# Optimization experiments

Measured on AMD Instinct MI355X. Metric: run time of the kernel, lower is better.

## Reference

```python
import jax, jax.numpy as jnp
from jax import lax
import numpy as np

VOCAB, E, H, T = 8000, 300, 75, 6  # H = hidden_dim//2 per direction
B, S = 256, 512
START, STOP = 4, 5
NEG = -10000.0


def setup_inputs() -> dict:
    key = jax.random.key(0)
    ks = jax.random.split(key, 16)
    sc = 0.1  # keep activations in sane range
    trans = jax.random.normal(ks[14], (T, T), jnp.float32)
    trans = trans.at[START, :].set(NEG).at[:, STOP].set(NEG)
    return {
        "sentence": jax.random.randint(ks[0], (B, S), 0, VOCAB),
        "tags": jax.random.randint(ks[1], (B, S), 0, 4),  # only B/I/E/S gold tags
        "embedding": jax.random.normal(ks[2], (VOCAB, E), jnp.float32),
        "w_ih_f": sc * jax.random.normal(ks[3], (4 * H, E), jnp.float32),
        "w_hh_f": sc * jax.random.normal(ks[4], (4 * H, H), jnp.float32),
        "b_ih_f": sc * jax.random.normal(ks[5], (4 * H,), jnp.float32),
        "b_hh_f": sc * jax.random.normal(ks[6], (4 * H,), jnp.float32),
        "w_ih_b": sc * jax.random.normal(ks[7], (4 * H, E), jnp.float32),
        "w_hh_b": sc * jax.random.normal(ks[8], (4 * H, H), jnp.float32),
        "b_ih_b": sc * jax.random.normal(ks[9], (4 * H,), jnp.float32),
        "b_hh_b": sc * jax.random.normal(ks[10], (4 * H,), jnp.float32),
        "h0": jax.random.normal(ks[11], (2, B, H), jnp.float32),
        "c0": jax.random.normal(ks[12], (2, B, H), jnp.float32),
        "w_out": sc * jax.random.normal(ks[13], (T, 2 * H), jnp.float32),
        "b_out": sc * jax.random.normal(ks[15], (T,), jnp.float32),
        "transitions": trans,
    }


def _lstm_dir(xg, w_hh, h0, c0, reverse):
    # xg: [S, B, 4H] precomputed input gates; PyTorch gate order i, f, g, o
    def step(carry, g):
        h, c = carry
        gates = g + h @ w_hh.T
        i, f, gg, o = jnp.split(gates, 4, axis=-1)
        c = jax.nn.sigmoid(f) * c + jax.nn.sigmoid(i) * jnp.tanh(gg)
        h = jax.nn.sigmoid(o) * jnp.tanh(c)
        return (h, c), h

    _, hs = lax.scan(step, (h0, c0), xg, reverse=reverse)
    return hs  # [S, B, H]


def reference(sentence, tags, embedding, w_ih_f, w_hh_f, b_ih_f, b_hh_f,
              w_ih_b, w_hh_b, b_ih_b, b_hh_b, h0, c0, w_out, b_out, transitions):
    # --- BiLSTM features ---
    embeds = embedding[sentence].transpose(1, 0, 2)  # [S, B, E]
    xg_f = embeds @ w_ih_f.T + (b_ih_f + b_hh_f)
    xg_b = embeds @ w_ih_b.T + (b_ih_b + b_hh_b)
    hf = _lstm_dir(xg_f, w_hh_f, h0[0], c0[0], reverse=False)
    hb = _lstm_dir(xg_b, w_hh_b, h0[1], c0[1], reverse=True)
    lstm_out = jnp.concatenate([hf, hb], axis=-1)  # [S, B, 2H]
    feats = lstm_out @ w_out.T + b_out  # [S, B, T]

    # --- CRF forward algorithm (log partition) ---
    alpha0 = jnp.full((feats.shape[1], T), NEG, feats.dtype).at[:, START].set(0.0)

    def crf_step(alpha, feat):
        # alpha_new[b, j] = logsumexp_i(alpha[b, i] + trans[j, i] + feat[b, j])
        alpha = jax.nn.logsumexp(
            alpha[:, None, :] + transitions[None, :, :] + feat[:, :, None], axis=2)
        return alpha, None

    alpha, _ = lax.scan(crf_step, alpha0, feats)
    forward_score = jax.nn.logsumexp(alpha + transitions[STOP][None, :], axis=1)  # [B]

    # --- gold path score ---
    tags_ext = jnp.concatenate(
        [jnp.full((tags.shape[0], 1), START, tags.dtype), tags], axis=1)  # [B, S+1]
    trans_sc = transitions[tags_ext[:, 1:], tags_ext[:, :-1]].sum(axis=1)  # [B]
    feats_bt = feats.transpose(1, 0, 2)  # [B, S, T]
    emit_sc = jnp.take_along_axis(feats_bt, tags[:, :, None], axis=2)[..., 0].sum(axis=1)
    gold_score = trans_sc + emit_sc + transitions[STOP, tags[:, -1]]

    return forward_score - gold_score  # [B] per-sentence CRF NLL
```

## Files before the change

kernel.cpp:

```cpp
#include <hip/hip_runtime.h>
#include <stdint.h>

#define VOCABN 8000
#define EE     300
#define HH     75
#define G4     300
#define TT     6
#define BB     256
#define SS     512
#define STARTT 4
#define STOPT  5
#define NEGV   (-10000.0f)
#define NCH    16
#define CHL    32

typedef __fp16 fp16x2 __attribute__((ext_vector_type(2)));
typedef __fp16 f16x8 __attribute__((ext_vector_type(8)));
typedef float f32x4 __attribute__((ext_vector_type(4)));
typedef unsigned int u32;

__device__ __forceinline__ float sigf(float x){
  return __builtin_amdgcn_rcpf(1.0f + __expf(-x));
}
__device__ __forceinline__ float tanhf_(float x){
  return __builtin_fmaf(__builtin_amdgcn_rcpf(1.0f + __expf(-2.0f * x)), 2.0f, -1.0f);
}
__device__ __forceinline__ float pk2(float a, float b){
  fp16x2 r = __builtin_amdgcn_cvt_pkrtz(a, b);
  return __builtin_bit_cast(float, r);
}
__device__ __forceinline__ float dot2pk(float a, float b, float c){
  asm("v_dot2_f32_f16 %0, %1, %2, %0" : "+v"(c) : "v"(a), "v"(b));
  return c;
}
__device__ __forceinline__ void sync_lds(){
  __builtin_amdgcn_sched_barrier(0);
  asm volatile("s_waitcnt lgkmcnt(0)" ::: "memory");
  __builtin_amdgcn_s_barrier();
  __builtin_amdgcn_sched_barrier(0);
}

__global__ __launch_bounds__(256) void k_gemm(
    const float* __restrict__ emb, const float* __restrict__ w_ih_f,
    const float* __restrict__ w_ih_b,
    const float* __restrict__ b_ih_f, const float* __restrict__ b_hh_f,
    const float* __restrict__ b_ih_b, const float* __restrict__ b_hh_b,
    float* __restrict__ vxg){
  __shared__ alignas(16) __fp16 bfrag[19 * 64 * 8];
  __shared__ float bias_sh[304];
  const int bx = blockIdx.x;
  const int dir = bx / 125;
  const int vblk = bx % 125;
  const int v0 = vblk * 64;
  const int tid = threadIdx.x;
  const int w = tid >> 6, lane = tid & 63;
  const int bb = lane & 15, q = lane >> 4;
  const float* wdir = dir ? w_ih_b : w_ih_f;

  for (int g = tid; g < 304; g += 256){
    float bi = 0.f;
    if (g < G4){
      int gs = (g & 3) * 75 + (g >> 2);
      bi = dir ? (b_ih_b[gs] + b_hh_b[gs]) : (b_ih_f[gs] + b_hh_f[gs]);
    }
    bias_sh[g] = bi;
  }
  if (tid < 16){
    int col = 12 + (tid & 3), qq = tid >> 2;
    *(u32*)&bfrag[(18 * 64 + qq * 16 + col) * 8]     = 0;
    *(u32*)&bfrag[(18 * 64 + qq * 16 + col) * 8 + 2] = 0;
    *(u32*)&bfrag[(18 * 64 + qq * 16 + col) * 8 + 4] = 0;
    *(u32*)&bfrag[(18 * 64 + qq * 16 + col) * 8 + 6] = 0;
  }

  f32x4 acc[19];
  #pragma unroll
  for (int t = 0; t < 19; ++t) acc[t] = (f32x4){0.f, 0.f, 0.f, 0.f};

  const float* arow = emb + (size_t)(v0 + 16 * w + bb) * EE;
  const int rstage = tid >> 3;
  const int sub = tid & 7;

  for (int c = 0; c < 10; ++c){
    f16x8 afrag;
    const int kb = 32 * c + 8 * q;
    if (c < 9){
      float4 x0 = *(const float4*)(arow + kb);
      float4 x1 = *(const float4*)(arow + kb + 4);
      afrag[0] = (__fp16)x0.x; afrag[1] = (__fp16)x0.y;
      afrag[2] = (__fp16)x0.z; afrag[3] = (__fp16)x0.w;
      afrag[4] = (__fp16)x1.x; afrag[5] = (__fp16)x1.y;
      afrag[6] = (__fp16)x1.z; afrag[7] = (__fp16)x1.w;
    } else {
      #pragma unroll
      for (int j = 0; j < 8; ++j)
        afrag[j] = (kb + j < EE) ? (__fp16)arow[kb + j] : (__fp16)0.f;
    }

    __syncthreads();
    for (int r0 = 0; r0 < 300; r0 += 32){
      int r = r0 + rstage;
      if (r < 300){
        int gsrc2 = (r & 3) * 75 + (r >> 2);
        const float* wr = wdir + (size_t)gsrc2 * EE;
        int e0 = 32 * c + 4 * sub;
        float4 xv;
        if (e0 + 3 < EE) xv = *(const float4*)(wr + e0);
        else {
          xv.x = (e0     < EE) ? wr[e0]     : 0.f;
          xv.y = (e0 + 1 < EE) ? wr[e0 + 1] : 0.f;
          xv.z = (e0 + 2 < EE) ? wr[e0 + 2] : 0.f;
          xv.w = (e0 + 3 < EE) ? wr[e0 + 3] : 0.f;
        }
        fp16x2 lo = __builtin_amdgcn_cvt_pkrtz(xv.x, xv.y);
        fp16x2 hi = __builtin_amdgcn_cvt_pkrtz(xv.z, xv.w);
        int t2 = r >> 4, col = r & 15;
        int qq = sub >> 1, j = 4 * (sub & 1);
        u32* dst = (u32*)&bfrag[(t2 * 64 + qq * 16 + col) * 8 + j];
        dst[0] = __builtin_bit_cast(u32, lo);
        dst[1] = __builtin_bit_cast(u32, hi);
      }
    }
    __syncthreads();

    #pragma unroll
    for (int t = 0; t < 19; ++t){
      f16x8 bf = *(const f16x8*)&bfrag[(t * 64 + lane) * 8];
      asm("v_mfma_f32_16x16x32_f16 %0, %1, %2, %0"
          : "+v"(acc[t]) : "v"(afrag), "v"(bf));
    }
  }

  const size_t obase = (size_t)dir * VOCABN * G4;
  #pragma unroll
  for (int t = 0; t < 19; ++t){
    int g = 16 * t + bb;
    if (g < G4){
      float bi = bias_sh[g];
      #pragma unroll
      for (int r = 0; r < 4; ++r){
        int v = v0 + 16 * w + 4 * q + r;
        vxg[obase + (size_t)v * G4 + g] = acc[t][r] + bi;
      }
    }
  }
}

__global__ __launch_bounds__(640) void k_lstm(
    const int* __restrict__ sentence, const float* __restrict__ vxg,
    const float* __restrict__ w_hh_f, const float* __restrict__ w_hh_b,
    const float* __restrict__ h0, const float* __restrict__ c0,
    const float* __restrict__ w_out, const float* __restrict__ b_out,
    float* __restrict__ featsF, float* __restrict__ featsB){
  __shared__ int tok_sh[SS * 16];
  __shared__ alignas(16) __fp16 hfrag[2][12 * 16 * 8];
  const int bx = blockIdx.x;
  const int dir = bx >> 4, group = bx & 15;
  const int t = threadIdx.x;
  const int w = t >> 6, lane = t & 63;
  const int bb = lane & 15, q = lane >> 4;
  const int T0 = 2 * w, T1 = 2 * w + 1;
  const int rbA = 16 * T0 + 4 * q, rbB = 16 * T1 + 4 * q;
  const int hA = rbA >> 2, hB = rbB >> 2;
  const int bglob = group * 16 + bb;
  const int wiA = w * 128 + bb * 8 + q;
  const int wiB = w * 128 + bb * 8 + 4 + q;

  for (int i = t; i < 2 * 12 * 16 * 4; i += 640) ((u32*)hfrag)[i] = 0;
  for (int i = t; i < 16 * SS; i += 640){
    int bq = i >> 9, s = i & 511;
    tok_sh[s * 16 + ((bq + s) & 15)] = sentence[(size_t)(group * 16 + bq) * SS + s];
  }
  __syncthreads();

  const float* whh = dir ? w_hh_b : w_hh_f;
  f16x8 a00, a01, a02, a10, a11, a12;
  #define BUILD_A(dst, T, c) { \
    int m = 16 * (T) + bb; int kb = 32 * (c) + 8 * q; \
    _Pragma("unroll") \
    for (int j = 0; j < 8; ++j){ \
      int kk = kb + j; float wv = 0.f; \
      if (kk < HH){ \
        if (m < 300) wv = whh[((m & 3) * 75 + (m >> 2)) * HH + kk]; \
        else if (m < 306) wv = w_out[(m - 300) * (2 * HH) + dir * HH + kk]; \
      } \
      dst[j] = (__fp16)wv; } }
  BUILD_A(a00, T0, 0) BUILD_A(a01, T0, 1) BUILD_A(a02, T0, 2)
  BUILD_A(a10, T1, 0) BUILD_A(a11, T1, 1) BUILD_A(a12, T1, 2)

  float cA = 0.f, cB = 0.f;
  if (hA < HH){
    cA = c0[((size_t)dir * BB + bglob) * HH + hA];
    hfrag[0][wiA] = (__fp16)h0[((size_t)dir * BB + bglob) * HH + hA];
  }
  if (hB < HH){
    cB = c0[((size_t)dir * BB + bglob) * HH + hB];
    hfrag[0][wiB] = (__fp16)h0[((size_t)dir * BB + bglob) * HH + hB];
  }
  const float bo0 = dir ? 0.f : b_out[0], bo1 = dir ? 0.f : b_out[1];
  const float bo2 = dir ? 0.f : b_out[2], bo3 = dir ? 0.f : b_out[3];
  const float bo4 = dir ? 0.f : b_out[4], bo5 = dir ? 0.f : b_out[5];
  __syncthreads();

  const float* vx = vxg + (size_t)dir * VOCABN * G4;
  float* feats = dir ? featsB : featsF;
  const float4 zf4 = {0.f, 0.f, 0.f, 0.f};

#define LOADXG(d0, d1, kstep) { \
    if ((kstep) < SS){ \
      int sr_ = dir ? (SS - 1 - (kstep)) : (kstep); \
      int tk_ = tok_sh[sr_ * 16 + ((bb + sr_) & 15)]; \
      const float* base_ = vx + (size_t)tk_ * G4; \
      d0 = (hA < HH) ? *(const float4*)(base_ + rbA) : zf4; \
      d1 = (hB < HH) ? *(const float4*)(base_ + rbB) : zf4; \
    } else { d0 = zf4; d1 = zf4; } }

  float4 cur0, cur1, n10, n11, n20, n21, n30, n31, p0, p1;
  LOADXG(cur0, cur1, 0)
  LOADXG(n10, n11, 1)
  LOADXG(n20, n21, 2)
  LOADXG(n30, n31, 3)

  for (int k = 0; k <= SS; ++k){
    const __fp16* hq = hfrag[k & 1];
    f16x8 b0 = *(const f16x8*)&hq[(0 * 64 + lane) * 8];
    f16x8 b1 = *(const f16x8*)&hq[(1 * 64 + lane) * 8];
    f16x8 b2 = *(const f16x8*)&hq[(2 * 64 + lane) * 8];

    LOADXG(p0, p1, k + 4)

    f32x4 acc0 = {cur0.x, cur0.y, cur0.z, cur0.w};
    f32x4 acc1 = {cur1.x, cur1.y, cur1.z, cur1.w};
    asm("v_mfma_f32_16x16x32_f16 %0, %1, %2, %0" : "+v"(acc0) : "a"(a00), "v"(b0));
    asm("v_mfma_f32_16x16x32_f16 %0, %1, %2, %0" : "+v"(acc1) : "a"(a10), "v"(b0));
    asm("v_mfma_f32_16x16x32_f16 %0, %1, %2, %0" : "+v"(acc0) : "a"(a01), "v"(b1));
    asm("v_mfma_f32_16x16x32_f16 %0, %1, %2, %0" : "+v"(acc1) : "a"(a11), "v"(b1));
    asm("v_mfma_f32_16x16x32_f16 %0, %1, %2, %0" : "+v"(acc0) : "a"(a02), "v"(b2));
    asm("v_mfma_f32_16x16x32_f16 %0, %1, %2, %0" : "+v"(acc1) : "a"(a12), "v"(b2));

    __fp16* hw = hfrag[(k & 1) ^ 1];
    if (k < SS){
      if (hA < HH){
        float gi = acc0.x, gf = acc0.y, gg = acc0.z, go = acc0.w;
        cA = sigf(gf) * cA + sigf(gi) * tanhf_(gg);
        hw[wiA] = (__fp16)(sigf(go) * tanhf_(cA));
      }
      if (hB < HH){
        float gi = acc1.x, gf = acc1.y, gg = acc1.z, go = acc1.w;
        cB = sigf(gf) * cB + sigf(gi) * tanhf_(gg);
        hw[wiB] = (__fp16)(sigf(go) * tanhf_(cB));
      }
    }
    if (k >= 1){
      if (rbA == 300){
        int ps = dir ? (SS - k) : (k - 1);
        float* fb = feats + ((size_t)ps * BB + bglob) * TT;
        float2 v01 = {acc0.x + bo0, acc0.y + bo1};
        float2 v23 = {acc0.z + bo2, acc0.w + bo3};
        *(float2*)fb = v01;
        *(float2*)(fb + 2) = v23;
      }
      if (rbB == 304){
        int ps = dir ? (SS - k) : (k - 1);
        float* fb = feats + ((size_t)ps * BB + bglob) * TT;
        float2 v45 = {acc1.x + bo4, acc1.y + bo5};
        *(float2*)(fb + 4) = v45;
      }
    }
    cur0 = n10; cur1 = n11;
    n10 = n20;  n11 = n21;
    n20 = n30;  n21 = n31;
    n30 = p0;   n31 = p1;
    sync_lds();
  }
}

#define LOADSTAGE(X0,X1,X2,Y0,Y1,Y2, srow) do{ \
  int _r = (srow); if (_r >= SS) _r = 0; \
  const float2* _pF = (const float2*)(featsF + ((size_t)_r * BB + b) * TT); \
  const float2* _pB = (const float2*)(featsB + ((size_t)_r * BB + b) * TT); \
  X0 = _pF[0]; X1 = _pF[1]; X2 = _pF[2]; \
  Y0 = _pB[0]; Y1 = _pB[1]; Y2 = _pB[2]; }while(0)

#define ASTEP(X0,X1,X2,Y0,Y1,Y2, srow) do{ \
  float F0 = X0.x + Y0.x, F1 = X0.y + Y0.y, F2 = X1.x + Y1.x; \
  float F3 = X1.y + Y1.y, F4 = X2.x + Y2.x, F5 = X2.y + Y2.y; \
  float M = fmaxf(fmaxf(fmaxf(a0,a1),fmaxf(a2,a3)),fmaxf(a4,a5)); \
  float p01 = pk2(__expf(a0-M), __expf(a1-M)); \
  float p23 = pk2(__expf(a2-M), __expf(a3-M)); \
  float p45 = pk2(__expf(a4-M), __expf(a5-M)); \
  float s0 = dot2pk(p45, Tq2,  dot2pk(p23, Tq1,  dot2pk(p01, Tq0,  0.f))); \
  float s1 = dot2pk(p45, Tq5,  dot2pk(p23, Tq4,  dot2pk(p01, Tq3,  0.f))); \
  float s2 = dot2pk(p45, Tq8,  dot2pk(p23, Tq7,  dot2pk(p01, Tq6,  0.f))); \
  float s3 = dot2pk(p45, Tq11, dot2pk(p23, Tq10, dot2pk(p01, Tq9,  0.f))); \
  float s4 = dot2pk(p45, Tq14, dot2pk(p23, Tq13, dot2pk(p01, Tq12, 0.f))); \
  float s5 = dot2pk(p45, Tq17, dot2pk(p23, Tq16, dot2pk(p01, Tq15, 0.f))); \
  a0 = M + __logf(fmaxf(s0, 1e-37f)) + F0;  a1 = M + __logf(fmaxf(s1, 1e-37f)) + F1; \
  a2 = M + __logf(fmaxf(s2, 1e-37f)) + F2;  a3 = M + __logf(fmaxf(s3, 1e-37f)) + F3; \
  a4 = M + __logf(fmaxf(s4, 1e-37f)) + F4;  a5 = M + __logf(fmaxf(s5, 1e-37f)) + F5; \
  LOADSTAGE(X0,X1,X2,Y0,Y1,Y2, (srow) + 2); }while(0)

__global__ __launch_bounds__(256) void k_crf_scan(
    const float* __restrict__ featsF, const float* __restrict__ featsB,
    const float* __restrict__ trans, const int* __restrict__ tags,
    float* __restrict__ crfM, float* __restrict__ pgold){
  __shared__ float tr_sh[36];
  __shared__ u32 etp_sh[18];
  const int tid = threadIdx.x;
  if (tid < 36) tr_sh[tid] = trans[tid];
  if (tid < 18) etp_sh[tid] = __float_as_uint(
      pk2(__expf(trans[2 * tid]), __expf(trans[2 * tid + 1])));
  __syncthreads();
  const int bx = blockIdx.x;

  if (bx < 96){
    const int g = bx * 256 + tid;
    const int s0i = g % 6;
    const int c = (g / 6) % NCH;
    const int b = g / (6 * NCH);
    const int cbase = c * CHL;

    float Tq0=__int_as_float(etp_sh[0]),  Tq1=__int_as_float(etp_sh[1]),
          Tq2=__int_as_float(etp_sh[2]),  Tq3=__int_as_float(etp_sh[3]),
          Tq4=__int_as_float(etp_sh[4]),  Tq5=__int_as_float(etp_sh[5]),
          Tq6=__int_as_float(etp_sh[6]),  Tq7=__int_as_float(etp_sh[7]),
          Tq8=__int_as_float(etp_sh[8]),  Tq9=__int_as_float(etp_sh[9]),
          Tq10=__int_as_float(etp_sh[10]), Tq11=__int_as_float(etp_sh[11]),
          Tq12=__int_as_float(etp_sh[12]), Tq13=__int_as_float(etp_sh[13]),
          Tq14=__int_as_float(etp_sh[14]), Tq15=__int_as_float(etp_sh[15]),
          Tq16=__int_as_float(etp_sh[16]), Tq17=__int_as_float(etp_sh[17]);

    float a0 = (s0i == 0) ? 0.f : NEGV, a1 = (s0i == 1) ? 0.f : NEGV;
    float a2 = (s0i == 2) ? 0.f : NEGV, a3 = (s0i == 3) ? 0.f : NEGV;
    float a4 = (s0i == 4) ? 0.f : NEGV, a5 = (s0i == 5) ? 0.f : NEGV;

    float2 xA0,xA1,xA2,yA0,yA1,yA2, xB0,xB1,xB2,yB0,yB1,yB2;
    LOADSTAGE(xA0,xA1,xA2,yA0,yA1,yA2, cbase + 0);
    LOADSTAGE(xB0,xB1,xB2,yB0,yB1,yB2, cbase + 1);
    for (int s = 0; s < CHL; s += 2){
      ASTEP(xA0,xA1,xA2,yA0,yA1,yA2, cbase + s);
      ASTEP(xB0,xB1,xB2,yB0,yB1,yB2, cbase + s + 1);
    }
    float* mrow = crfM + ((size_t)(b * NCH + c) * 6 + s0i) * 6;
    mrow[0] = a0; mrow[1] = a1; mrow[2] = a2;
    mrow[3] = a3; mrow[4] = a4; mrow[5] = a5;
  } else {
    const int g2 = (bx - 96) * 256 + tid;
    const int b = g2 / NCH;
    const int c = g2 % NCH;
    const int* tg = tags + (size_t)b * SS + c * CHL;
    int prev = (c == 0) ? STARTT : tg[-1];
    float acc = 0.f;
    #pragma unroll 4
    for (int s = 0; s < CHL; ++s){
      int ct = tg[s];
      size_t fo = (size_t)(c * CHL + s) * BB * TT + (size_t)b * TT + ct;
      acc += tr_sh[ct * 6 + prev] + featsF[fo] + featsB[fo];
      prev = ct;
    }
    pgold[b * NCH + c] = acc;
  }
}

__global__ __launch_bounds__(64) void k_crf_comb(
    const float* __restrict__ crfM, const float* __restrict__ pgold,
    const float* __restrict__ trans, const int* __restrict__ tags,
    float* __restrict__ out){
  const int b = blockIdx.x * 64 + threadIdx.x;
  float v0 = NEGV, v1 = NEGV, v2 = NEGV, v3 = NEGV, v4 = 0.f, v5 = NEGV;
  for (int c = 0; c < NCH; ++c){
    const float* mb = crfM + (size_t)(b * NCH + c) * 36;
    float n[6];
    #pragma unroll
    for (int j = 0; j < 6; ++j){
      float t0 = v0 + mb[0 * 6 + j], t1 = v1 + mb[1 * 6 + j];
      float t2 = v2 + mb[2 * 6 + j], t3 = v3 + mb[3 * 6 + j];
      float t4 = v4 + mb[4 * 6 + j], t5 = v5 + mb[5 * 6 + j];
      float m = fmaxf(fmaxf(fmaxf(t0,t1),fmaxf(t2,t3)),fmaxf(t4,t5));
      float s = __expf(t0-m)+__expf(t1-m)+__expf(t2-m)
              + __expf(t3-m)+__expf(t4-m)+__expf(t5-m);
      n[j] = m + __logf(s);
    }
    v0 = n[0]; v1 = n[1]; v2 = n[2]; v3 = n[3]; v4 = n[4]; v5 = n[5];
  }
  float z0 = v0 + trans[30], z1 = v1 + trans[31], z2 = v2 + trans[32];
  float z3 = v3 + trans[33], z4 = v4 + trans[34], z5 = v5 + trans[35];
  float M2 = fmaxf(fmaxf(fmaxf(z0,z1),fmaxf(z2,z3)),fmaxf(z4,z5));
  float ss = __expf(z0-M2)+__expf(z1-M2)+__expf(z2-M2)
           + __expf(z3-M2)+__expf(z4-M2)+__expf(z5-M2);
  float fwd = M2 + __logf(ss);

  float gold = trans[STOPT * 6 + tags[(size_t)b * SS + SS - 1]];
  #pragma unroll
  for (int c = 0; c < NCH; ++c) gold += pgold[b * NCH + c];
  out[b] = fwd - gold;
}

extern "C" void kernel_launch(void* const* d_in, const int* in_sizes, int n_in,
                              void* d_out, int out_size, void* d_ws, size_t ws_size,
                              hipStream_t stream){
  const int*   sentence = (const int*)  d_in[0];
  const int*   tags     = (const int*)  d_in[1];
  const float* emb      = (const float*)d_in[2];
  const float* w_ih_f   = (const float*)d_in[3];
  const float* w_hh_f   = (const float*)d_in[4];
  const float* b_ih_f   = (const float*)d_in[5];
  const float* b_hh_f   = (const float*)d_in[6];
  const float* w_ih_b   = (const float*)d_in[7];
  const float* w_hh_b   = (const float*)d_in[8];
  const float* b_ih_b   = (const float*)d_in[9];
  const float* b_hh_b   = (const float*)d_in[10];
  const float* h0       = (const float*)d_in[11];
  const float* c0       = (const float*)d_in[12];
  const float* w_out    = (const float*)d_in[13];
  const float* b_out    = (const float*)d_in[14];
  const float* trans    = (const float*)d_in[15];
  float* out = (float*)d_out;

  float* ws = (float*)d_ws;
  float* vxg    = ws;
  float* featsF = vxg + (size_t)2 * VOCABN * G4;
  float* featsB = featsF + (size_t)SS * BB * TT;
  float* crfM   = featsB + (size_t)SS * BB * TT;
  float* pgold  = crfM + (size_t)BB * NCH * 36;

  k_gemm<<<2 * 125, 256, 0, stream>>>(emb, w_ih_f, w_ih_b,
                                      b_ih_f, b_hh_f, b_ih_b, b_hh_b, vxg);
  k_lstm<<<32, 640, 0, stream>>>(sentence, vxg, w_hh_f, w_hh_b, h0, c0, w_out, b_out,
                                 featsF, featsB);
  k_crf_scan<<<96 + 16, 256, 0, stream>>>(featsF, featsB, trans, tags, crfM, pgold);
  k_crf_comb<<<BB / 64, 64, 0, stream>>>(crfM, pgold, trans, tags, out);
}
```

Measured before the change: 467.6 us.

## Process two 16-sequence batch slices per LSTM block to interleave recurrences

Each LSTM block now handles 32 batch rows as two independent 16-row slices, so the grid drops from 32 to 16 blocks. The two recurrences interleave their MFMAs and gate math, which can hide MFMA and transcendental latency on the serial step chain. Token indices are stored as u16 to fit twice as many in LDS, and the xg prefetch depth falls from 4 steps to 2 to save registers. The risk is a longer per-step critical path (twice the MFMAs and activations per wave), fewer CUs in use, and more exposed global-load latency from the shallower prefetch.

Result: slower. 815.2 us (+74.3%).

```diff
diff --git a/kernel.cpp b/kernel.cpp
--- a/kernel.cpp
+++ b/kernel.cpp
@@ -18,6 +18,7 @@
 typedef __fp16 f16x8 __attribute__((ext_vector_type(8)));
 typedef float f32x4 __attribute__((ext_vector_type(4)));
 typedef unsigned int u32;
+typedef unsigned short u16;
 
 __device__ __forceinline__ float sigf(float x){
   return __builtin_amdgcn_rcpf(1.0f + __expf(-x));
@@ -152,24 +153,26 @@
     const float* __restrict__ h0, const float* __restrict__ c0,
     const float* __restrict__ w_out, const float* __restrict__ b_out,
     float* __restrict__ featsF, float* __restrict__ featsB){
-  __shared__ int tok_sh[SS * 16];
-  __shared__ alignas(16) __fp16 hfrag[2][12 * 16 * 8];
+  __shared__ u16 tok_sh[SS * 32];
+  __shared__ alignas(16) __fp16 hfrag[2][2][12 * 16 * 8];
   const int bx = blockIdx.x;
-  const int dir = bx >> 4, group = bx & 15;
+  const int dir = bx >> 3, group = bx & 7;
   const int t = threadIdx.x;
   const int w = t >> 6, lane = t & 63;
   const int bb = lane & 15, q = lane >> 4;
   const int T0 = 2 * w, T1 = 2 * w + 1;
   const int rbA = 16 * T0 + 4 * q, rbB = 16 * T1 + 4 * q;
   const int hA = rbA >> 2, hB = rbB >> 2;
-  const int bglob = group * 16 + bb;
+  const int bg0 = group * 32 + bb;
+  const int bg1 = group * 32 + 16 + bb;
   const int wiA = w * 128 + bb * 8 + q;
   const int wiB = w * 128 + bb * 8 + 4 + q;
 
-  for (int i = t; i < 2 * 12 * 16 * 4; i += 640) ((u32*)hfrag)[i] = 0;
-  for (int i = t; i < 16 * SS; i += 640){
+  for (int i = t; i < 2 * 2 * 12 * 16 * 4; i += 640) ((u32*)hfrag)[i] = 0;
+  for (int i = t; i < 32 * SS; i += 640){
     int bq = i >> 9, s = i & 511;
-    tok_sh[s * 16 + ((bq + s) & 15)] = sentence[(size_t)(group * 16 + bq) * SS + s];
+    tok_sh[s * 32 + ((bq + s) & 31)] =
+        (u16)sentence[(size_t)(group * 32 + bq) * SS + s];
   }
   __syncthreads();
 
@@ -188,14 +191,18 @@
   BUILD_A(a00, T0, 0) BUILD_A(a01, T0, 1) BUILD_A(a02, T0, 2)
   BUILD_A(a10, T1, 0) BUILD_A(a11, T1, 1) BUILD_A(a12, T1, 2)
 
-  float cA = 0.f, cB = 0.f;
+  float cA0 = 0.f, cB0 = 0.f, cA1 = 0.f, cB1 = 0.f;
   if (hA < HH){
-    cA = c0[((size_t)dir * BB + bglob) * HH + hA];
-    hfrag[0][wiA] = (__fp16)h0[((size_t)dir * BB + bglob) * HH + hA];
+    cA0 = c0[((size_t)dir * BB + bg0) * HH + hA];
+    cA1 = c0[((size_t)dir * BB + bg1) * HH + hA];
+    hfrag[0][0][wiA] = (__fp16)h0[((size_t)dir * BB + bg0) * HH + hA];
+    hfrag[0][1][wiA] = (__fp16)h0[((size_t)dir * BB + bg1) * HH + hA];
   }
   if (hB < HH){
-    cB = c0[((size_t)dir * BB + bglob) * HH + hB];
-    hfrag[0][wiB] = (__fp16)h0[((size_t)dir * BB + bglob) * HH + hB];
+    cB0 = c0[((size_t)dir * BB + bg0) * HH + hB];
+    cB1 = c0[((size_t)dir * BB + bg1) * HH + hB];
+    hfrag[0][0][wiB] = (__fp16)h0[((size_t)dir * BB + bg0) * HH + hB];
+    hfrag[0][1][wiB] = (__fp16)h0[((size_t)dir * BB + bg1) * HH + hB];
   }
   const float bo0 = dir ? 0.f : b_out[0], bo1 = dir ? 0.f : b_out[1];
   const float bo2 = dir ? 0.f : b_out[2], bo3 = dir ? 0.f : b_out[3];
@@ -206,71 +213,96 @@
   float* feats = dir ? featsB : featsF;
   const float4 zf4 = {0.f, 0.f, 0.f, 0.f};
 
-#define LOADXG(d0, d1, kstep) { \
+#define LOADXG2(dA0, dB0, dA1, dB1, kstep) { \
     if ((kstep) < SS){ \
       int sr_ = dir ? (SS - 1 - (kstep)) : (kstep); \
-      int tk_ = tok_sh[sr_ * 16 + ((bb + sr_) & 15)]; \
-      const float* base_ = vx + (size_t)tk_ * G4; \
-      d0 = (hA < HH) ? *(const float4*)(base_ + rbA) : zf4; \
-      d1 = (hB < HH) ? *(const float4*)(base_ + rbB) : zf4; \
-    } else { d0 = zf4; d1 = zf4; } }
-
-  float4 cur0, cur1, n10, n11, n20, n21, n30, n31, p0, p1;
-  LOADXG(cur0, cur1, 0)
-  LOADXG(n10, n11, 1)
-  LOADXG(n20, n21, 2)
-  LOADXG(n30, n31, 3)
+      int tk0_ = tok_sh[sr_ * 32 + ((bb + sr_) & 31)]; \
+      int tk1_ = tok_sh[sr_ * 32 + ((bb + 16 + sr_) & 31)]; \
+      const float* bs0_ = vx + (size_t)tk0_ * G4; \
+      const float* bs1_ = vx + (size_t)tk1_ * G4; \
+      dA0 = (hA < HH) ? *(const float4*)(bs0_ + rbA) : zf4; \
+      dB0 = (hB < HH) ? *(const float4*)(bs0_ + rbB) : zf4; \
+      dA1 = (hA < HH) ? *(const float4*)(bs1_ + rbA) : zf4; \
+      dB1 = (hB < HH) ? *(const float4*)(bs1_ + rbB) : zf4; \
+    } else { dA0 = zf4; dB0 = zf4; dA1 = zf4; dB1 = zf4; } }
+
+  float4 curA0, curB0, curA1, curB1, nxA0, nxB0, nxA1, nxB1;
+  float4 pA0, pB0, pA1, pB1;
+  LOADXG2(curA0, curB0, curA1, curB1, 0)
+  LOADXG2(nxA0, nxB0, nxA1, nxB1, 1)
 
   for (int k = 0; k <= SS; ++k){
-    const __fp16* hq = hfrag[k & 1];
-    f16x8 b0 = *(const f16x8*)&hq[(0 * 64 + lane) * 8];
-    f16x8 b1 = *(const f16x8*)&hq[(1 * 64 + lane) * 8];
-    f16x8 b2 = *(const f16x8*)&hq[(2 * 64 + lane) * 8];
-
-    LOADXG(p0, p1, k + 4)
-
-    f32x4 acc0 = {cur0.x, cur0.y, cur0.z, cur0.w};
-    f32x4 acc1 = {cur1.x, cur1.y, cur1.z, cur1.w};
-    asm("v_mfma_f32_16x16x32_f16 %0, %1, %2, %0" : "+v"(acc0) : "a"(a00), "v"(b0));
-    asm("v_mfma_f32_16x16x32_f16 %0, %1, %2, %0" : "+v"(acc1) : "a"(a10), "v"(b0));
-    asm("v_mfma_f32_16x16x32_f16 %0, %1, %2, %0" : "+v"(acc0) : "a"(a01), "v"(b1));
-    asm("v_mfma_f32_16x16x32_f16 %0, %1, %2, %0" : "+v"(acc1) : "a"(a11), "v"(b1));
-    asm("v_mfma_f32_16x16x32_f16 %0, %1, %2, %0" : "+v"(acc0) : "a"(a02), "v"(b2));
-    asm("v_mfma_f32_16x16x32_f16 %0, %1, %2, %0" : "+v"(acc1) : "a"(a12), "v"(b2));
-
-    __fp16* hw = hfrag[(k & 1) ^ 1];
+    const __fp16* hq0 = hfrag[k & 1][0];
+    const __fp16* hq1 = hfrag[k & 1][1];
+    f16x8 b0s0 = *(const f16x8*)&hq0[(0 * 64 + lane) * 8];
+    f16x8 b0s1 = *(const f16x8*)&hq1[(0 * 64 + lane) * 8];
+    f16x8 b1s0 = *(const f16x8*)&hq0[(1 * 64 + lane) * 8];
+    f16x8 b1s1 = *(const f16x8*)&hq1[(1 * 64 + lane) * 8];
+    f16x8 b2s0 = *(const f16x8*)&hq0[(2 * 64 + lane) * 8];
+    f16x8 b2s1 = *(const f16x8*)&hq1[(2 * 64 + lane) * 8];
+
+    LOADXG2(pA0, pB0, pA1, pB1, k + 2)
+
+    f32x4 accA0 = {curA0.x, curA0.y, curA0.z, curA0.w};
+    f32x4 accA1 = {curA1.x, curA1.y, curA1.z, curA1.w};
+    f32x4 accB0 = {curB0.x, curB0.y, curB0.z, curB0.w};
+    f32x4 accB1 = {curB1.x, curB1.y, curB1.z, curB1.w};
+    asm("v_mfma_f32_16x16x32_f16 %0, %1, %2, %0" : "+v"(accA0) : "a"(a00), "v"(b0s0));
+    asm("v_mfma_f32_16x16x32_f16 %0, %1, %2, %0" : "+v"(accA1) : "a"(a00), "v"(b0s1));
+    asm("v_mfma_f32_16x16x32_f16 %0, %1, %2, %0" : "+v"(accB0) : "a"(a10), "v"(b0s0));
+    asm("v_mfma_f32_16x16x32_f16 %0, %1, %2, %0" : "+v"(accB1) : "a"(a10), "v"(b0s1));
+    asm("v_mfma_f32_16x16x32_f16 %0, %1, %2, %0" : "+v"(accA0) : "a"(a01), "v"(b1s0));
+    asm("v_mfma_f32_16x16x32_f16 %0, %1, %2, %0" : "+v"(accA1) : "a"(a01), "v"(b1s1));
+    asm("v_mfma_f32_16x16x32_f16 %0, %1, %2, %0" : "+v"(accB0) : "a"(a11), "v"(b1s0));
+    asm("v_mfma_f32_16x16x32_f16 %0, %1, %2, %0" : "+v"(accB1) : "a"(a11), "v"(b1s1));
+    asm("v_mfma_f32_16x16x32_f16 %0, %1, %2, %0" : "+v"(accA0) : "a"(a02), "v"(b2s0));
+    asm("v_mfma_f32_16x16x32_f16 %0, %1, %2, %0" : "+v"(accA1) : "a"(a02), "v"(b2s1));
+    asm("v_mfma_f32_16x16x32_f16 %0, %1, %2, %0" : "+v"(accB0) : "a"(a12), "v"(b2s0));
+    asm("v_mfma_f32_16x16x32_f16 %0, %1, %2, %0" : "+v"(accB1) : "a"(a12), "v"(b2s1));
+
+    __fp16* hw0 = hfrag[(k & 1) ^ 1][0];
+    __fp16* hw1 = hfrag[(k & 1) ^ 1][1];
     if (k < SS){
       if (hA < HH){
-        float gi = acc0.x, gf = acc0.y, gg = acc0.z, go = acc0.w;
-        cA = sigf(gf) * cA + sigf(gi) * tanhf_(gg);
-        hw[wiA] = (__fp16)(sigf(go) * tanhf_(cA));
+        { float gi = accA0.x, gf = accA0.y, gg = accA0.z, go = accA0.w;
+          cA0 = sigf(gf) * cA0 + sigf(gi) * tanhf_(gg);
+          hw0[wiA] = (__fp16)(sigf(go) * tanhf_(cA0)); }
+        { float gi = accA1.x, gf = accA1.y, gg = accA1.z, go = accA1.w;
+          cA1 = sigf(gf) * cA1 + sigf(gi) * tanhf_(gg);
+          hw1[wiA] = (__fp16)(sigf(go) * tanhf_(cA1)); }
       }
       if (hB < HH){
-        float gi = acc1.x, gf = acc1.y, gg = acc1.z, go = acc1.w;
-        cB = sigf(gf) * cB + sigf(gi) * tanhf_(gg);
-        hw[wiB] = (__fp16)(sigf(go) * tanhf_(cB));
+        { float gi = accB0.x, gf = accB0.y, gg = accB0.z, go = accB0.w;
+          cB0 = sigf(gf) * cB0 + sigf(gi) * tanhf_(gg);
+          hw0[wiB] = (__fp16)(sigf(go) * tanhf_(cB0)); }
+        { float gi = accB1.x, gf = accB1.y, gg = accB1.z, go = accB1.w;
+          cB1 = sigf(gf) * cB1 + sigf(gi) * tanhf_(gg);
+          hw1[wiB] = (__fp16)(sigf(go) * tanhf_(cB1)); }
       }
     }
     if (k >= 1){
+      int ps = dir ? (SS - k) : (k - 1);
       if (rbA == 300){
-        int ps = dir ? (SS - k) : (k - 1);
-        float* fb = feats + ((size_t)ps * BB + bglob) * TT;
-        float2 v01 = {acc0.x + bo0, acc0.y + bo1};
-        float2 v23 = {acc0.z + bo2, acc0.w + bo3};
-        *(float2*)fb = v01;
-        *(float2*)(fb + 2) = v23;
+        float* fb0 = feats + ((size_t)ps * BB + bg0) * TT;
+        float* fb1 = feats + ((size_t)ps * BB + bg1) * TT;
+        float2 u01 = {accA0.x + bo0, accA0.y + bo1};
+        float2 u23 = {accA0.z + bo2, accA0.w + bo3};
+        *(float2*)fb0 = u01; *(float2*)(fb0 + 2) = u23;
+        float2 v01 = {accA1.x + bo0, accA1.y + bo1};
+        float2 v23 = {accA1.z + bo2, accA1.w + bo3};
+        *(float2*)fb1 = v01; *(float2*)(fb1 + 2) = v23;
       }
       if (rbB == 304){
-        int ps = dir ? (SS - k) : (k - 1);
-        float* fb = feats + ((size_t)ps * BB + bglob) * TT;
-        float2 v45 = {acc1.x + bo4, acc1.y + bo5};
-        *(float2*)(fb + 4) = v45;
-      }
-    }
-    cur0 = n10; cur1 = n11;
-    n10 = n20;  n11 = n21;
-    n20 = n30;  n21 = n31;
-    n30 = p0;   n31 = p1;
+        float* fb0 = feats + ((size_t)ps * BB + bg0) * TT;
+        float* fb1 = feats + ((size_t)ps * BB + bg1) * TT;
+        float2 u45 = {accB0.x + bo4, accB0.y + bo5};
+        *(float2*)(fb0 + 4) = u45;
+        float2 v45 = {accB1.x + bo4, accB1.y + bo5};
+        *(float2*)(fb1 + 4) = v45;
+      }
+    }
+    curA0 = nxA0; curB0 = nxB0; curA1 = nxA1; curB1 = nxB1;
+    nxA0 = pA0;  nxB0 = pB0;  nxA1 = pA1;  nxB1 = pB1;
     sync_lds();
   }
 }
@@ -426,7 +458,7 @@
 
   k_gemm<<<2 * 125, 256, 0, stream>>>(emb, w_ih_f, w_ih_b,
                                       b_ih_f, b_hh_f, b_ih_b, b_hh_b, vxg);
-  k_lstm<<<32, 640, 0, stream>>>(sentence, vxg, w_hh_f, w_hh_b, h0, c0, w_out, b_out,
+  k_lstm<<<16, 640, 0, stream>>>(sentence, vxg, w_hh_f, w_hh_b, h0, c0, w_out, b_out,
                                  featsF, featsB);
   k_crf_scan<<<96 + 16, 256, 0, stream>>>(featsF, featsB, trans, tags, crfM, pgold);
   k_crf_comb<<<BB / 64, 64, 0, stream>>>(crfM, pgold, trans, tags, out);
```
